# Optimization experiments

Hardware: AMD Instinct MI355X
Metric: run time of the kernel (lower is better)

Reference implementation:

```python
import jax, jax.numpy as jnp
import numpy as np


def setup_inputs() -> dict:
    key = jax.random.key(0)
    ks = jax.random.split(key, 8)
    B, N, D = 8, 2048, 128
    s = 1.0 / float(np.sqrt(D))
    node = jax.random.normal(ks[0], (B, N, D), dtype=jnp.float32)
    node_mask = jax.random.randint(ks[1], (B, N), 0, 2, dtype=jnp.int32)
    punctuation_graph = jax.random.randint(ks[2], (B, N, N), 0, 2, dtype=jnp.int32)
    w_nw = jax.random.uniform(ks[3], (1, D), jnp.float32, -s, s)
    b_nw = jax.random.uniform(ks[4], (1,), jnp.float32, -s, s)
    w_self = jax.random.uniform(ks[5], (D, D), jnp.float32, -s, s)
    b_self = jax.random.uniform(ks[6], (D,), jnp.float32, -s, s)
    w_punct = jax.random.uniform(ks[7], (D, D), jnp.float32, -s, s)
    return {"node": node, "node_mask": node_mask, "punctuation_graph": punctuation_graph,
            "w_nw": w_nw, "b_nw": b_nw, "w_self": w_self, "b_self": b_self,
            "w_punct": w_punct, "iteration_steps": 2}


def reference(node, node_mask, punctuation_graph, w_nw, b_nw, w_self, b_self, w_punct, iteration_steps):
    B, N, D = node.shape
    # dd_graph = mask outer product with zeroed diagonal; graph = dd_graph * punctuation_graph
    eye = jnp.eye(N, dtype=punctuation_graph.dtype)
    dd = node_mask[:, None, :] * node_mask[:, :, None] * (1 - eye)[None, :, :]  # [B,N,N]
    graph = dd * punctuation_graph  # [B,N,N] int, binary
    nbr_num = graph.sum(-1)  # [B,N]
    # replace_masked_values(nbr_num, nbr_num>=1, 1): nodes with no neighbors get denom 1
    nbr_f = jnp.where(nbr_num >= 1, nbr_num.astype(node.dtype), jnp.asarray(1.0, node.dtype))
    gmask = graph > 0
    weights = []
    x = node
    for _ in range(iteration_steps):  # small fixed step count
        dw = jax.nn.sigmoid(jnp.einsum('bnd,od->bno', x, w_nw) + b_nw)[..., 0]  # [B,N]
        weights.append(dw)
        self_info = jnp.einsum('bnd,ed->bne', x, w_self) + b_self  # [B,N,D]
        info_p = jnp.einsum('bnd,ed->bne', x, w_punct)  # [B,N,D]
        # node_weight[b,i,j] = dw[b,j] where graph[b,i,j] else 0
        nw = jnp.where(gmask, dw[:, None, :], jnp.asarray(0.0, x.dtype))  # [B,N,N]
        agg = jnp.einsum('bnm,bmd->bnd', nw, info_p) / nbr_f[..., None]
        x = jax.nn.relu(self_info + agg)
    all_weight = jnp.stack(weights, axis=1)  # [B, steps, N]
    return x, all_weight
```

## Files before the change

kernel.cpp:

```cpp
#include <hip/hip_runtime.h>
#include <hip/hip_bf16.h>

#define BB 8
#define NN 2048
#define DD 128

typedef __attribute__((ext_vector_type(8))) __bf16 bf16x8;
typedef __attribute__((ext_vector_type(4))) float f32x4;
typedef __attribute__((ext_vector_type(4))) int   i32x4;

static __device__ __forceinline__ unsigned short f2bf(float f) {
    union { float f; unsigned u; } v; v.f = f;
    unsigned r = (v.u + 0x7FFFu + ((v.u >> 16) & 1u)) >> 16;
    return (unsigned short)r;
}
static __device__ __forceinline__ float bf2f(unsigned short b) {
    union { unsigned u; float f; } v; v.u = ((unsigned)b) << 16;
    return v.f;
}

template <bool PRECONV>
static __device__ __forceinline__ void kernB_body(
    int n0, const float* __restrict__ x,
    const float* __restrict__ w_nw,  const float* __restrict__ b_nw,
    const void* __restrict__ wself_p, const float* __restrict__ b_self,
    const void* __restrict__ wpunct_p,
    float* __restrict__ si_out,
    unsigned short* __restrict__ yne_out,
    unsigned short* __restrict__ yT_out,
    float* __restrict__ aw_out)
{
    __shared__ unsigned short xt[64*32];
    __shared__ unsigned short wst[128*32];
    __shared__ unsigned short wpt[128*32];
    __shared__ float wnw_l[DD];
    __shared__ float red[256];
    __shared__ float dw_l[64];
    __shared__ unsigned short ytl[128*72];

    const int t  = threadIdx.x;
    const int b  = n0 >> 11;
    const int nb = n0 & (NN - 1);

    if (t < DD) wnw_l[t] = w_nw[t];
    __syncthreads();

    const int wave = t >> 6, lane = t & 63;
    const int wm = wave >> 1, wn = wave & 1;
    const int quad = lane >> 4, l16 = lane & 15;

    const int n_loc = t >> 2, dq = t & 3;
    const int we = t >> 1,   wh = t & 1;

    f32x4 accs[2][4] = {}; f32x4 accp[2][4] = {};
    float dwpart = 0.f;

    #pragma unroll
    for (int kk = 0; kk < 4; ++kk) {
        const int k0 = kk * 32;
        {
            const float* xs = x + (size_t)(n0 + n_loc) * DD + k0 + dq * 8;
            f32x4 a = *(const f32x4*)xs;
            f32x4 c = *(const f32x4*)(xs + 4);
            const float* wv = &wnw_l[k0 + dq * 8];
            dwpart += a.x*wv[0] + a.y*wv[1] + a.z*wv[2] + a.w*wv[3]
                    + c.x*wv[4] + c.y*wv[5] + c.z*wv[6] + c.w*wv[7];
            unsigned q0 = f2bf(a.x) | ((unsigned)f2bf(a.y) << 16);
            unsigned q1 = f2bf(a.z) | ((unsigned)f2bf(a.w) << 16);
            unsigned q2 = f2bf(c.x) | ((unsigned)f2bf(c.y) << 16);
            unsigned q3 = f2bf(c.z) | ((unsigned)f2bf(c.w) << 16);
            i32x4 pw = {(int)q0,(int)q1,(int)q2,(int)q3};
            *(i32x4*)&xt[n_loc*32 + dq*8] = pw;
        }
        if (PRECONV) {
            const unsigned short* s1 = (const unsigned short*)wself_p  + (size_t)we * DD + k0 + wh*16;
            const unsigned short* s2 = (const unsigned short*)wpunct_p + (size_t)we * DD + k0 + wh*16;
            i32x4 a0 = *(const i32x4*)s1;
            i32x4 a1 = *(const i32x4*)(s1 + 8);
            *(i32x4*)&wst[we*32 + wh*16]     = a0;
            *(i32x4*)&wst[we*32 + wh*16 + 8] = a1;
            i32x4 c0 = *(const i32x4*)s2;
            i32x4 c1 = *(const i32x4*)(s2 + 8);
            *(i32x4*)&wpt[we*32 + wh*16]     = c0;
            *(i32x4*)&wpt[we*32 + wh*16 + 8] = c1;
        } else {
            const float* s1 = (const float*)wself_p  + (size_t)we * DD + k0 + wh*16;
            const float* s2 = (const float*)wpunct_p + (size_t)we * DD + k0 + wh*16;
            f32x4 a0 = *(const f32x4*)s1;      f32x4 a1 = *(const f32x4*)(s1+4);
            f32x4 a2 = *(const f32x4*)(s1+8);  f32x4 a3 = *(const f32x4*)(s1+12);
            unsigned q0 = f2bf(a0.x) | ((unsigned)f2bf(a0.y)<<16);
            unsigned q1 = f2bf(a0.z) | ((unsigned)f2bf(a0.w)<<16);
            unsigned q2 = f2bf(a1.x) | ((unsigned)f2bf(a1.y)<<16);
            unsigned q3 = f2bf(a1.z) | ((unsigned)f2bf(a1.w)<<16);
            unsigned q4 = f2bf(a2.x) | ((unsigned)f2bf(a2.y)<<16);
            unsigned q5 = f2bf(a2.z) | ((unsigned)f2bf(a2.w)<<16);
            unsigned q6 = f2bf(a3.x) | ((unsigned)f2bf(a3.y)<<16);
            unsigned q7 = f2bf(a3.z) | ((unsigned)f2bf(a3.w)<<16);
            i32x4 pw0 = {(int)q0,(int)q1,(int)q2,(int)q3};
            i32x4 pw1 = {(int)q4,(int)q5,(int)q6,(int)q7};
            *(i32x4*)&wst[we*32 + wh*16]     = pw0;
            *(i32x4*)&wst[we*32 + wh*16 + 8] = pw1;
            f32x4 c0 = *(const f32x4*)s2;      f32x4 c1 = *(const f32x4*)(s2+4);
            f32x4 c2 = *(const f32x4*)(s2+8);  f32x4 c3 = *(const f32x4*)(s2+12);
            unsigned r0 = f2bf(c0.x) | ((unsigned)f2bf(c0.y)<<16);
            unsigned r1 = f2bf(c0.z) | ((unsigned)f2bf(c0.w)<<16);
            unsigned r2 = f2bf(c1.x) | ((unsigned)f2bf(c1.y)<<16);
            unsigned r3 = f2bf(c1.z) | ((unsigned)f2bf(c1.w)<<16);
            unsigned r4 = f2bf(c2.x) | ((unsigned)f2bf(c2.y)<<16);
            unsigned r5 = f2bf(c2.z) | ((unsigned)f2bf(c2.w)<<16);
            unsigned r6 = f2bf(c3.x) | ((unsigned)f2bf(c3.y)<<16);
            unsigned r7 = f2bf(c3.z) | ((unsigned)f2bf(c3.w)<<16);
            i32x4 pv0 = {(int)r0,(int)r1,(int)r2,(int)r3};
            i32x4 pv1 = {(int)r4,(int)r5,(int)r6,(int)r7};
            *(i32x4*)&wpt[we*32 + wh*16]     = pv0;
            *(i32x4*)&wpt[we*32 + wh*16 + 8] = pv1;
        }
        __syncthreads();
        bf16x8 af[2], bs[4], bp[4];
        #pragma unroll
        for (int mt = 0; mt < 2; ++mt)
            af[mt] = *(const bf16x8*)&xt[(wm*32 + mt*16 + l16)*32 + quad*8];
        #pragma unroll
        for (int nt = 0; nt < 4; ++nt) {
            const int er = wn*64 + nt*16 + l16;
            bs[nt] = *(const bf16x8*)&wst[er*32 + quad*8];
            bp[nt] = *(const bf16x8*)&wpt[er*32 + quad*8];
        }
        #pragma unroll
        for (int mt = 0; mt < 2; ++mt)
            #pragma unroll
            for (int nt = 0; nt < 4; ++nt) {
                accs[mt][nt] = __builtin_amdgcn_mfma_f32_16x16x32_bf16(af[mt], bs[nt], accs[mt][nt], 0, 0, 0);
                accp[mt][nt] = __builtin_amdgcn_mfma_f32_16x16x32_bf16(af[mt], bp[nt], accp[mt][nt], 0, 0, 0);
            }
        __syncthreads();
    }

    red[t] = dwpart;
    __syncthreads();
    if (t < 64) {
        float s = red[4*t] + red[4*t+1] + red[4*t+2] + red[4*t+3] + b_nw[0];
        float dv = 1.f / (1.f + __expf(-s));
        dw_l[t] = dv;
        aw_out[(size_t)b * 2 * NN + nb + t] = dv;
    }
    __syncthreads();

    #pragma unroll
    for (int mt = 0; mt < 2; ++mt) {
        #pragma unroll
        for (int nt = 0; nt < 4; ++nt) {
            const int e = wn*64 + nt*16 + l16;
            const float bsv = b_self[e];
            #pragma unroll
            for (int r = 0; r < 4; ++r) {
                const int nl = wm*32 + mt*16 + quad*4 + r;
                const size_t idx = (size_t)(n0 + nl) * DD + e;
                si_out[idx] = accs[mt][nt][r] + bsv;
                const float yv = dw_l[nl] * accp[mt][nt][r];
                const unsigned short ub = f2bf(yv);
                yne_out[idx] = ub;
                ytl[e*72 + nl] = ub;
            }
        }
    }
    __syncthreads();
    {
        const int e = t >> 1, half = t & 1;
        const i32x4* src = (const i32x4*)&ytl[e*72 + half*32];
        i32x4 v0 = src[0], v1 = src[1], v2 = src[2], v3 = src[3];
        i32x4* dst = (i32x4*)(yT_out + (size_t)(b*DD + e) * NN + nb + half*32);
        dst[0] = v0; dst[1] = v1; dst[2] = v2; dst[3] = v3;
    }
}

__global__ __launch_bounds__(256) void kern0(
    const int* __restrict__ punct, const int* __restrict__ mask,
    const float* __restrict__ node,
    const float* __restrict__ w_nw, const float* __restrict__ b_nw,
    const float* __restrict__ w_self, const float* __restrict__ b_self,
    const float* __restrict__ w_punct,
    unsigned* __restrict__ pk, float* __restrict__ scale_g, float* __restrict__ pdm_g,
    unsigned short* __restrict__ wsb, unsigned short* __restrict__ wpb,
    float* __restrict__ si, unsigned short* __restrict__ yne,
    unsigned short* __restrict__ yT, float* __restrict__ aw)
{
    const int bid = blockIdx.x;
    const int t = threadIdx.x;

    if (bid < 256) {
        kernB_body<false>(bid * 64, node, w_nw, b_nw, w_self, b_self, w_punct,
                          si, yne, yT, aw);
        return;
    }
    if (bid < 272) {
        const int cb = bid - 256;
        const float* src = (cb < 8) ? w_self : w_punct;
        unsigned short* dst = (cb < 8) ? wsb : wpb;
        const size_t i0 = (size_t)(cb & 7) * 2048 + (size_t)t * 8;
        f32x4 a = *(const f32x4*)(src + i0);
        f32x4 c = *(const f32x4*)(src + i0 + 4);
        unsigned q0 = f2bf(a.x) | ((unsigned)f2bf(a.y) << 16);
        unsigned q1 = f2bf(a.z) | ((unsigned)f2bf(a.w) << 16);
        unsigned q2 = f2bf(c.x) | ((unsigned)f2bf(c.y) << 16);
        unsigned q3 = f2bf(c.z) | ((unsigned)f2bf(c.w) << 16);
        i32x4 pw = {(int)q0, (int)q1, (int)q2, (int)q3};
        *(i32x4*)(dst + i0) = pw;
        return;
    }

    const int wave = t >> 6, lane = t & 63;
    const int row_g = (bid - 272) * 4 + wave;
    const int b = row_g >> 11;
    const int i = row_g & (NN - 1);

    const int* prow = punct + (size_t)row_g * NN;
    const int* mrow = mask + (size_t)b * NN;

    unsigned pk0 = 0, pk1 = 0;
    int acc = 0;
    #pragma unroll 4
    for (int w = 0; w < 32; ++w) {
        const int col = w * 64 + lane;
        const int p = prow[col];
        const int m = mrow[col];
        const int pred = (p & m) & 1;
        unsigned long long bal = __ballot(pred);
        if (lane == w) { pk0 = (unsigned)bal; pk1 = (unsigned)(bal >> 32); }
        acc += pred + ((col == i ? pred : 0) << 16);
    }
    #pragma unroll
    for (int o = 32; o > 0; o >>= 1) acc += __shfl_xor(acc, o, 64);

    if (lane < 32) {
        uint2 w2; w2.x = pk0; w2.y = pk1;
        *(uint2*)(pk + (size_t)row_g * 64 + 2 * lane) = w2;
    }
    if (lane == 0) {
        const int nall = acc & 0xFFFF;
        const int pdm  = acc >> 16;
        const int mi   = mrow[i];
        const int nbr  = nall - pdm;
        scale_g[row_g] = mi ? 1.f / (float)(nbr < 1 ? 1 : nbr) : 0.f;
        pdm_g[row_g]   = (float)pdm;
    }
}

__global__ __launch_bounds__(256) void kernB1(
    const float* __restrict__ x,
    const unsigned short* __restrict__ wsb, const unsigned short* __restrict__ wpb,
    const float* __restrict__ w_nw, const float* __restrict__ b_nw,
    const float* __restrict__ b_self,
    float* __restrict__ si, unsigned short* __restrict__ yne,
    unsigned short* __restrict__ yT, float* __restrict__ aw1)
{
    kernB_body<true>(blockIdx.x * 64, x, w_nw, b_nw, wsb, b_self, wpb,
                     si, yne, yT, aw1);
}

__global__ __launch_bounds__(256) void kernC(
    const unsigned* __restrict__ pk,
    const float* __restrict__ scale_g, const float* __restrict__ pdm_g,
    const unsigned short* __restrict__ yT,
    const float* __restrict__ si,
    const unsigned short* __restrict__ yne,
    float* __restrict__ x_out)
{
    __shared__ unsigned pPk[64 * 68];
    __shared__ float scale_l[64];
    __shared__ float pdm_l[64];

    const int t  = threadIdx.x;
    const int b  = blockIdx.x & 7;
    const int i0 = (blockIdx.x >> 3) * 64;
    const size_t rg0 = (size_t)b * NN + i0;

    #pragma unroll
    for (int r = 0; r < 4; ++r) {
        const int u   = r * 256 + t;
        const int row = u >> 4;
        const int wq  = (u & 15) * 4;
        i32x4 v = *(const i32x4*)(pk + (rg0 + row) * 64 + wq);
        *(i32x4*)&pPk[row * 68 + wq] = v;
    }
    if (t < 64) {
        scale_l[t] = scale_g[rg0 + t];
        pdm_l[t]   = pdm_g[rg0 + t];
    }
    __syncthreads();

    const int wn = t >> 6, lane = t & 63;
    const int quad = lane >> 4, l16 = lane & 15;
    const unsigned short* yTb = yT + (size_t)b * DD * NN;

    f32x4 acc[4][2] = {};

    #pragma unroll 4
    for (int kk = 0; kk < 64; ++kk) {
        bf16x8 bfr[2];
        #pragma unroll
        for (int nt = 0; nt < 2; ++nt) {
            const int e = wn*32 + nt*16 + l16;
            bfr[nt] = *(const bf16x8*)(yTb + (size_t)e * NN + kk*32 + quad*8);
        }
        bf16x8 af[4];
        #pragma unroll
        for (int mt = 0; mt < 4; ++mt) {
            const unsigned w = pPk[(mt*16 + l16) * 68 + kk];
            const unsigned by = (w >> (quad * 8)) & 0xFFu;
            i32x4 ex;
            ex.x = ((by &   1u) ? 0x3F80 : 0) | ((by &   2u) ? 0x3F800000 : 0);
            ex.y = ((by &   4u) ? 0x3F80 : 0) | ((by &   8u) ? 0x3F800000 : 0);
            ex.z = ((by &  16u) ? 0x3F80 : 0) | ((by &  32u) ? 0x3F800000 : 0);
            ex.w = ((by &  64u) ? 0x3F80 : 0) | ((by & 128u) ? 0x3F800000 : 0);
            union { i32x4 i; bf16x8 h; } cv; cv.i = ex;
            af[mt] = cv.h;
        }
        #pragma unroll
        for (int mt = 0; mt < 4; ++mt)
            #pragma unroll
            for (int nt = 0; nt < 2; ++nt)
                acc[mt][nt] = __builtin_amdgcn_mfma_f32_16x16x32_bf16(af[mt], bfr[nt], acc[mt][nt], 0, 0, 0);
    }

    #pragma unroll
    for (int mt = 0; mt < 4; ++mt) {
        #pragma unroll
        for (int nt = 0; nt < 2; ++nt) {
            const int e = wn*32 + nt*16 + l16;
            #pragma unroll
            for (int r = 0; r < 4; ++r) {
                const int row = mt*16 + quad*4 + r;
                const size_t idx = (rg0 + row) * DD + e;
                const float yv = bf2f(yne[idx]);
                float v = si[idx] + scale_l[row] * (acc[mt][nt][r] - pdm_l[row] * yv);
                x_out[idx] = fmaxf(v, 0.f);
            }
        }
    }
}

extern "C" void kernel_launch(void* const* d_in, const int* in_sizes, int n_in,
                              void* d_out, int out_size, void* d_ws, size_t ws_size,
                              hipStream_t stream) {
    const float* node   = (const float*)d_in[0];
    const int*   mask   = (const int*)  d_in[1];
    const int*   punct  = (const int*)  d_in[2];
    const float* w_nw   = (const float*)d_in[3];
    const float* b_nw   = (const float*)d_in[4];
    const float* w_self = (const float*)d_in[5];
    const float* b_self = (const float*)d_in[6];
    const float* w_punct= (const float*)d_in[7];

    float* xout = (float*)d_out;
    float* aw   = xout + (size_t)BB * NN * DD;

    char* w = (char*)d_ws;
    float*          si   = (float*)w;
    unsigned short* yne  = (unsigned short*)(w + (8u  << 20));
    unsigned short* yT   = (unsigned short*)(w + (12u << 20));
    unsigned*       pk   = (unsigned*)(w + (16u << 20));
    float*          scl  = (float*)(w + (20u << 20));
    float*          pdm  = (float*)(w + (20u << 20) + (64u << 10));
    unsigned short* wsb  = (unsigned short*)(w + (21u << 20));
    unsigned short* wpb  = (unsigned short*)(w + (21u << 20) + (32u << 10));

    dim3 blk(256);
    kern0<<<dim3(4368), blk, 0, stream>>>(punct, mask, node, w_nw, b_nw,
                                          w_self, b_self, w_punct,
                                          pk, scl, pdm, wsb, wpb,
                                          si, yne, yT, aw);
    kernC<<<dim3(256), blk, 0, stream>>>(pk, scl, pdm, yT, si, yne, xout);
    kernB1<<<dim3(256), blk, 0, stream>>>(xout, wsb, wpb, w_nw, b_nw, b_self,
                                          si, yne, yT, aw + NN);
    kernC<<<dim3(256), blk, 0, stream>>>(pk, scl, pdm, yT, si, yne, xout);
}
```

Before: 299.7 us.

## Split fused prologue kernel and vectorize graph bit-packing with 128-bit loads

The fused prologue kernel is split into a graph bit-packing kernel and a separate first-step projection kernel. The packing kernel now has each wave handle two rows with 128-bit loads. The mask row is cached once as a 32-bit register bitmask instead of being reloaded per element, and nibbles are assembled into words through shuffles rather than per-column ballots. The goal is to cut load instructions and redundant mask traffic when streaming the large int32 graph, at the cost of one extra kernel launch and lost overlap between the projection GEMM and the packing work.

```diff
diff --git a/kernel.cpp b/kernel.cpp
--- a/kernel.cpp
+++ b/kernel.cpp
@@ -17,6 +17,84 @@
 static __device__ __forceinline__ float bf2f(unsigned short b) {
     union { unsigned u; float f; } v; v.u = ((unsigned)b) << 16;
     return v.f;
+}
+
+__global__ __launch_bounds__(256) void kernP2(
+    const int* __restrict__ punct, const int* __restrict__ mask,
+    const float* __restrict__ w_self, const float* __restrict__ w_punct,
+    unsigned* __restrict__ pk, float* __restrict__ scale_g, float* __restrict__ pdm_g,
+    unsigned short* __restrict__ wsb, unsigned short* __restrict__ wpb)
+{
+    const int bid = blockIdx.x;
+    const int t = threadIdx.x;
+
+    if (bid >= 2048) {
+        const int cb = bid - 2048;
+        const float* src = (cb < 8) ? w_self : w_punct;
+        unsigned short* dst = (cb < 8) ? wsb : wpb;
+        const size_t i0 = (size_t)(cb & 7) * 2048 + (size_t)t * 8;
+        f32x4 a = *(const f32x4*)(src + i0);
+        f32x4 c = *(const f32x4*)(src + i0 + 4);
+        unsigned q0 = f2bf(a.x) | ((unsigned)f2bf(a.y) << 16);
+        unsigned q1 = f2bf(a.z) | ((unsigned)f2bf(a.w) << 16);
+        unsigned q2 = f2bf(c.x) | ((unsigned)f2bf(c.y) << 16);
+        unsigned q3 = f2bf(c.z) | ((unsigned)f2bf(c.w) << 16);
+        i32x4 pw = {(int)q0, (int)q1, (int)q2, (int)q3};
+        *(i32x4*)(dst + i0) = pw;
+        return;
+    }
+
+    const int wave = t >> 6, lane = t & 63;
+    const int row0 = bid * 8 + wave * 2;
+    const int b = row0 >> 11;
+    const int* mrow = mask + (size_t)b * NN;
+
+    unsigned mreg = 0;
+    #pragma unroll
+    for (int g = 0; g < 8; ++g) {
+        i32x4 m = *(const i32x4*)(mrow + g * 256 + lane * 4);
+        unsigned nib = (m.x & 1) | ((m.y & 1) << 1) | ((m.z & 1) << 2) | ((m.w & 1) << 3);
+        mreg |= nib << (4 * g);
+    }
+
+    #pragma unroll
+    for (int r = 0; r < 2; ++r) {
+        const int row = row0 + r;
+        const int i = row & (NN - 1);
+        const int* prow = punct + (size_t)row * NN;
+        unsigned* pkrow = pk + (size_t)row * 64;
+
+        int acc = 0;
+        #pragma unroll
+        for (int g = 0; g < 8; ++g) {
+            i32x4 v = *(const i32x4*)(prow + g * 256 + lane * 4);
+            unsigned nib = (v.x & 1) | ((v.y & 1) << 1) | ((v.z & 1) << 2) | ((v.w & 1) << 3);
+            nib &= (mreg >> (4 * g)) & 0xFu;
+            acc += __popc(nib);
+            if (((i >> 8) == g) && (((i >> 2) & 63) == lane))
+                acc += (int)((nib >> (i & 3)) & 1u) << 16;
+            unsigned p1 = __shfl_xor(nib, 1, 64);
+            unsigned lo = (lane & 1) ? p1 : nib, hi = (lane & 1) ? nib : p1;
+            unsigned by = lo | (hi << 4);
+            unsigned p2 = __shfl_xor(by, 2, 64);
+            lo = (lane & 2) ? p2 : by; hi = (lane & 2) ? by : p2;
+            unsigned hf = lo | (hi << 8);
+            unsigned p4 = __shfl_xor(hf, 4, 64);
+            lo = (lane & 4) ? p4 : hf; hi = (lane & 4) ? hf : p4;
+            unsigned wd = lo | (hi << 16);
+            if ((lane & 7) == 0) pkrow[g * 8 + (lane >> 3)] = wd;
+        }
+        #pragma unroll
+        for (int o = 32; o > 0; o >>= 1) acc += __shfl_xor(acc, o, 64);
+        if (lane == 0) {
+            const int nall = acc & 0xFFFF;
+            const int pdm  = acc >> 16;
+            const int mi   = mrow[i];
+            const int nbr  = nall - pdm;
+            scale_g[row] = mi ? 1.f / (float)(nbr < 1 ? 1 : nbr) : 0.f;
+            pdm_g[row]   = (float)pdm;
+        }
+    }
 }
 
 template <bool PRECONV>
@@ -174,76 +252,16 @@
     }
 }
 
-__global__ __launch_bounds__(256) void kern0(
-    const int* __restrict__ punct, const int* __restrict__ mask,
+__global__ __launch_bounds__(256) void kernB0(
     const float* __restrict__ node,
     const float* __restrict__ w_nw, const float* __restrict__ b_nw,
     const float* __restrict__ w_self, const float* __restrict__ b_self,
     const float* __restrict__ w_punct,
-    unsigned* __restrict__ pk, float* __restrict__ scale_g, float* __restrict__ pdm_g,
-    unsigned short* __restrict__ wsb, unsigned short* __restrict__ wpb,
     float* __restrict__ si, unsigned short* __restrict__ yne,
     unsigned short* __restrict__ yT, float* __restrict__ aw)
 {
-    const int bid = blockIdx.x;
-    const int t = threadIdx.x;
-
-    if (bid < 256) {
-        kernB_body<false>(bid * 64, node, w_nw, b_nw, w_self, b_self, w_punct,
-                          si, yne, yT, aw);
-        return;
-    }
-    if (bid < 272) {
-        const int cb = bid - 256;
-        const float* src = (cb < 8) ? w_self : w_punct;
-        unsigned short* dst = (cb < 8) ? wsb : wpb;
-        const size_t i0 = (size_t)(cb & 7) * 2048 + (size_t)t * 8;
-        f32x4 a = *(const f32x4*)(src + i0);
-        f32x4 c = *(const f32x4*)(src + i0 + 4);
-        unsigned q0 = f2bf(a.x) | ((unsigned)f2bf(a.y) << 16);
-        unsigned q1 = f2bf(a.z) | ((unsigned)f2bf(a.w) << 16);
-        unsigned q2 = f2bf(c.x) | ((unsigned)f2bf(c.y) << 16);
-        unsigned q3 = f2bf(c.z) | ((unsigned)f2bf(c.w) << 16);
-        i32x4 pw = {(int)q0, (int)q1, (int)q2, (int)q3};
-        *(i32x4*)(dst + i0) = pw;
-        return;
-    }
-
-    const int wave = t >> 6, lane = t & 63;
-    const int row_g = (bid - 272) * 4 + wave;
-    const int b = row_g >> 11;
-    const int i = row_g & (NN - 1);
-
-    const int* prow = punct + (size_t)row_g * NN;
-    const int* mrow = mask + (size_t)b * NN;
-
-    unsigned pk0 = 0, pk1 = 0;
-    int acc = 0;
-    #pragma unroll 4
-    for (int w = 0; w < 32; ++w) {
-        const int col = w * 64 + lane;
-        const int p = prow[col];
-        const int m = mrow[col];
-        const int pred = (p & m) & 1;
-        unsigned long long bal = __ballot(pred);
-        if (lane == w) { pk0 = (unsigned)bal; pk1 = (unsigned)(bal >> 32); }
-        acc += pred + ((col == i ? pred : 0) << 16);
-    }
-    #pragma unroll
-    for (int o = 32; o > 0; o >>= 1) acc += __shfl_xor(acc, o, 64);
-
-    if (lane < 32) {
-        uint2 w2; w2.x = pk0; w2.y = pk1;
-        *(uint2*)(pk + (size_t)row_g * 64 + 2 * lane) = w2;
-    }
-    if (lane == 0) {
-        const int nall = acc & 0xFFFF;
-        const int pdm  = acc >> 16;
-        const int mi   = mrow[i];
-        const int nbr  = nall - pdm;
-        scale_g[row_g] = mi ? 1.f / (float)(nbr < 1 ? 1 : nbr) : 0.f;
-        pdm_g[row_g]   = (float)pdm;
-    }
+    kernB_body<false>(blockIdx.x * 64, node, w_nw, b_nw, w_self, b_self, w_punct,
+                      si, yne, yT, aw);
 }
 
 __global__ __launch_bounds__(256) void kernB1(
@@ -366,10 +384,10 @@
     unsigned short* wpb  = (unsigned short*)(w + (21u << 20) + (32u << 10));
 
     dim3 blk(256);
-    kern0<<<dim3(4368), blk, 0, stream>>>(punct, mask, node, w_nw, b_nw,
-                                          w_self, b_self, w_punct,
-                                          pk, scl, pdm, wsb, wpb,
-                                          si, yne, yT, aw);
+    kernP2<<<dim3(2064), blk, 0, stream>>>(punct, mask, w_self, w_punct,
+                                           pk, scl, pdm, wsb, wpb);
+    kernB0<<<dim3(256), blk, 0, stream>>>(node, w_nw, b_nw, w_self, b_self,
+                                          w_punct, si, yne, yT, aw);
     kernC<<<dim3(256), blk, 0, stream>>>(pk, scl, pdm, yT, si, yne, xout);
     kernB1<<<dim3(256), blk, 0, stream>>>(xout, wsb, wpb, w_nw, b_nw, b_self,
                                           si, yne, yT, aw + NN);
```

New measurement: 289.0 us. -3.6%, faster.
